# Performance work log

Measured on AMD Instinct MI355X. Metric: run time of the kernel, lower is better.

## Reference

```python
import jax, jax.numpy as jnp
import numpy as np

N_NODES = 10000
N_EDGES = 160000
HIDDEN = 64
NUM_RBF = 32
Q_DIM = 8
CUTOFF_UPPER = 5.0


def silu(x):
    return x * jax.nn.sigmoid(x)


def tensor_norm(X):
    # X: [n, 3, 3, H] -> [n, H] (Frobenius norm squared over the 3x3 dims)
    return (X * X).sum(axis=(1, 2))


def decompose_tensor(X):
    # X: [n, 3, 3, H] -> I: [n, H] (trace/3), A: antisym [n,3,3,H], S: sym traceless [n,3,3,H]
    eye = jnp.eye(3, dtype=X.dtype)[None, :, :, None]
    I = jnp.einsum('naah->nh', X) / 3.0
    Xt = X.transpose(0, 2, 1, 3)
    A = 0.5 * (X - Xt)
    S = 0.5 * (X + Xt) - I[:, None, None, :] * eye
    return I, A, S


def compose_tensor(I, A, S):
    eye = jnp.eye(3, dtype=A.dtype)[None, :, :, None]
    return I[:, None, None, :] * eye + A + S


def tmm(P, Q):
    # 3x3 matmul per (atom, channel): [n,3,3,H] x [n,3,3,H] -> [n,3,3,H]
    return jnp.einsum('nach,ncbh->nabh', P, Q)


def setup_inputs() -> dict:
    key = jax.random.key(0)
    ks = jax.random.split(key, 16)
    H = HIDDEN
    inp = {
        'X': jax.random.normal(ks[0], (N_NODES, 3, 3, H), jnp.float32),
        'charges': jax.random.normal(ks[1], (N_NODES, Q_DIM), jnp.float32),
        'edge_weight': jax.random.uniform(ks[2], (N_EDGES,), jnp.float32) * CUTOFF_UPPER,
        'edge_attr': jax.random.normal(ks[3], (N_EDGES, NUM_RBF), jnp.float32),
        'edge_index': jax.random.randint(ks[4], (2, N_EDGES), 0, N_NODES, jnp.int32),
    }
    d_in = NUM_RBF + 2 * Q_DIM
    inp['Ws1'] = jax.random.normal(ks[5], (d_in, H), jnp.float32) / np.sqrt(d_in).astype(np.float32)
    inp['bs1'] = jnp.zeros((H,), jnp.float32)
    inp['Ws2'] = jax.random.normal(ks[6], (H, 2 * H), jnp.float32) / np.sqrt(H).astype(np.float32)
    inp['bs2'] = jnp.zeros((2 * H,), jnp.float32)
    inp['Ws3'] = jax.random.normal(ks[7], (2 * H, 3 * H), jnp.float32) / np.sqrt(2 * H).astype(np.float32)
    inp['bs3'] = jnp.zeros((3 * H,), jnp.float32)
    for i in range(6):
        inp['Wt%d' % i] = jax.random.normal(ks[8 + i], (H, H), jnp.float32) / np.sqrt(H).astype(np.float32)
    return inp


def reference(X, charges, edge_weight, edge_attr, Ws1, bs1, Ws2, bs2, Ws3, bs3,
              Wt0, Wt1, Wt2, Wt3, Wt4, Wt5, edge_index):
    H = HIDDEN
    n = X.shape[0]
    row, col = edge_index[0], edge_index[1]
    # cosine cutoff (cutoff_lower = 0)
    C = 0.5 * (jnp.cos(edge_weight * (jnp.pi / CUTOFF_UPPER)) + 1.0)
    C = C * (edge_weight < CUTOFF_UPPER).astype(X.dtype)
    # edge scalar MLP on [rbf, q_i, q_j]
    h = jnp.concatenate([edge_attr, charges[row], charges[col]], axis=-1)
    h = silu(h @ Ws1 + bs1)
    h = silu(h @ Ws2 + bs2)
    h = silu(h @ Ws3 + bs3)
    w = (h * C[:, None]).reshape(h.shape[0], 3, H)  # [E, 3, H]
    # normalize node tensors
    X = X / (tensor_norm(X) + 1.0)[:, None, None, :]
    I, A, S = decompose_tensor(X)
    I = I @ Wt0
    A = A @ Wt1
    S = S @ Wt2
    Y = compose_tensor(I, A, S)
    # message passing: gather I/A/S at source (edge_index[1]), weight per component, scatter-add at dest (edge_index[0])
    eye = jnp.eye(3, dtype=X.dtype)[None, :, :, None]
    msg_e = ((w[:, 0] * I[col])[:, None, None, :] * eye
             + w[:, 1][:, None, None, :] * A[col]
             + w[:, 2][:, None, None, :] * S[col])  # [E, 3, 3, H]
    msg = jax.ops.segment_sum(msg_e, row, num_segments=n)  # [n, 3, 3, H]
    # O(3): C = msg @ Y + Y @ msg (3x3 matmul per channel)
    Cm = tmm(msg, Y) + tmm(Y, msg)
    I2, A2, S2 = decompose_tensor(Cm)
    normp1 = tensor_norm(Cm) + 1.0
    I2 = I2 / normp1
    A2 = A2 / normp1[:, None, None, :]
    S2 = S2 / normp1[:, None, None, :]
    I2 = I2 @ Wt3
    A2 = A2 @ Wt4
    S2 = S2 @ Wt5
    dX = compose_tensor(I2, A2, S2)
    return X + dX + tmm(dX, dX)
```

## Files before the change

### kernel.cpp

```cpp
#include <hip/hip_runtime.h>
#include <math.h>

#define HD 64

typedef _Float16 half8 __attribute__((ext_vector_type(8)));
typedef _Float16 half4v __attribute__((ext_vector_type(4)));
typedef float floatx4 __attribute__((ext_vector_type(4)));

__device__ __forceinline__ float silu_f(float x) {
    return x * __builtin_amdgcn_rcpf(1.0f + __expf(-x));
}

__global__ __launch_bounds__(256) void pre_wconv(
    const float* __restrict__ X,
    const float* __restrict__ Wt0, const float* __restrict__ Wt1, const float* __restrict__ Wt2,
    float* __restrict__ Tn, _Float16* __restrict__ TnH, int N, int nbPre,
    const float* __restrict__ Ws1, const float* __restrict__ Ws2, const float* __restrict__ Ws3,
    _Float16* __restrict__ W1f, _Float16* __restrict__ W2f, _Float16* __restrict__ W3f)
{
    if (blockIdx.x >= nbPre) {
        int id = (blockIdx.x - nbPre) * 256 + threadIdx.x;
        if (id < 4096) {
            int i = id & 7, l = (id >> 3) & 63, t = id >> 9;
            int s = t >> 2, nt = t & 3;
            int k = s * 32 + (l >> 4) * 8 + i;
            int n = nt * 16 + (l & 15);
            W1f[id] = (k < 48) ? (_Float16)Ws1[k * 64 + n] : (_Float16)0.f;
        } else if (id < 4096 + 8192) {
            int j = id - 4096;
            int i = j & 7, l = (j >> 3) & 63, t = j >> 9;
            int s = t >> 3, nt = t & 7;
            int k = s * 32 + (l >> 4) * 8 + i;
            int n = nt * 16 + (l & 15);
            W2f[j] = (_Float16)Ws2[k * 128 + n];
        } else if (id < 4096 + 8192 + 24576) {
            int j = id - 4096 - 8192;
            int i = j & 7, l = (j >> 3) & 63, t = j >> 9;
            int s = t / 12, nt = t % 12;
            int k = s * 32 + (l >> 4) * 8 + i;
            int n = nt * 16 + (l & 15);
            W3f[j] = (_Float16)Ws3[k * 192 + n];
        }
        return;
    }

    int sub = threadIdx.x >> 6;
    int h = threadIdx.x & 63;
    int n = blockIdx.x * 4 + sub;
    int nn = (n < N) ? n : (N - 1);

    const float* Xb = X + (size_t)nn * 9 * HD + h;
    float x[9];
    float nrm = 0.f;
#pragma unroll
    for (int i = 0; i < 9; ++i) { x[i] = Xb[i * HD]; nrm += x[i] * x[i]; }
    float inv = 1.0f / (nrm + 1.0f);
#pragma unroll
    for (int i = 0; i < 9; ++i) x[i] *= inv;

    float I0 = (x[0] + x[4] + x[8]) * (1.0f / 3.0f);
    __shared__ float comp[4][10][HD];
    comp[sub][0][h] = I0;
    comp[sub][1][h] = 0.5f * (x[1] - x[3]);
    comp[sub][2][h] = 0.5f * (x[2] - x[6]);
    comp[sub][3][h] = 0.5f * (x[5] - x[7]);
    comp[sub][4][h] = x[0] - I0;
    comp[sub][5][h] = 0.5f * (x[1] + x[3]);
    comp[sub][6][h] = 0.5f * (x[2] + x[6]);
    comp[sub][7][h] = x[4] - I0;
    comp[sub][8][h] = 0.5f * (x[5] + x[7]);
    comp[sub][9][h] = x[8] - I0;
    __syncthreads();
    float acc[10];
#pragma unroll
    for (int i = 0; i < 10; ++i) acc[i] = 0.f;
    for (int k = 0; k < HD; ++k) {
        float w0 = Wt0[k * HD + h];
        float w1 = Wt1[k * HD + h];
        float w2 = Wt2[k * HD + h];
        acc[0] += comp[sub][0][k] * w0;
        acc[1] += comp[sub][1][k] * w1;
        acc[2] += comp[sub][2][k] * w1;
        acc[3] += comp[sub][3][k] * w1;
#pragma unroll
        for (int j = 0; j < 6; ++j) acc[4 + j] += comp[sub][4 + j][k] * w2;
    }
    if (n < N) {
        float* tp = Tn + (size_t)n * 640 + h;
        _Float16* th = TnH + (size_t)n * 640 + h;
#pragma unroll
        for (int i = 0; i < 10; ++i) {
            tp[i * 64] = acc[i];
            th[i * 64] = (_Float16)acc[i];
        }
    }
}

__global__ __launch_bounds__(256) void count_kernel(
    const int* __restrict__ edge_index, int* __restrict__ cnt, int E)
{
    int e = blockIdx.x * 256 + threadIdx.x;
    if (e < E) atomicAdd(&cnt[edge_index[e]], 1);
}

__global__ __launch_bounds__(1024) void scanA(
    const int* __restrict__ cnt, int* __restrict__ offs, int* __restrict__ partial, int N)
{
    __shared__ int wsum[16];
    int tid = threadIdx.x, wid = tid >> 6, lane = tid & 63;
    int i = blockIdx.x * 1024 + tid;
    int v = (i < N) ? cnt[i] : 0;
    int s = v;
#pragma unroll
    for (int d = 1; d < 64; d <<= 1) {
        int t = __shfl_up(s, d, 64);
        if (lane >= d) s += t;
    }
    if (lane == 63) wsum[wid] = s;
    __syncthreads();
    if (tid == 0) {
        int run = 0;
#pragma unroll
        for (int w = 0; w < 16; ++w) { int t = wsum[w]; wsum[w] = run; run += t; }
        partial[blockIdx.x] = run;
    }
    __syncthreads();
    if (i < N) offs[i] = wsum[wid] + s - v;
}

__global__ __launch_bounds__(256) void scanC(
    int* __restrict__ offs, const int* __restrict__ partial, int* __restrict__ curs,
    int N, int E)
{
    int i = blockIdx.x * 256 + threadIdx.x;
    if (i < N) {
        int b = i >> 10;
        int basev = 0;
        for (int w = 0; w < b; ++w) basev += partial[w];
        int o = offs[i] + basev;
        offs[i] = o;
        curs[i] = o;
    }
    if (i == 0) offs[N] = E;
}

__global__ __launch_bounds__(256) void place_kernel(
    const int* __restrict__ edge_index, int* __restrict__ curs,
    int* __restrict__ rank, int* __restrict__ colP, int E)
{
    int e = blockIdx.x * 256 + threadIdx.x;
    if (e < E) {
        int p = atomicAdd(&curs[edge_index[e]], 1);
        rank[e] = p;
        colP[p] = edge_index[E + e];
    }
}

__global__ __launch_bounds__(256, 6) void mlp_mfma(
    const float* __restrict__ edge_attr, const float* __restrict__ charges,
    const float* __restrict__ edge_weight, const int* __restrict__ edge_index,
    const int* __restrict__ rank,
    const _Float16* __restrict__ W1f, const float* __restrict__ bs1,
    const _Float16* __restrict__ W2f, const float* __restrict__ bs2,
    const _Float16* __restrict__ W3f, const float* __restrict__ bs3,
    _Float16* __restrict__ bufH, int E)
{
    __shared__ __align__(16) _Float16 act[4][16][136];
    __shared__ float cvsS[4][16];
    __shared__ int rankSS[4][16];

    int tid = threadIdx.x;
    int wv = tid >> 6, l = tid & 63;
    int base = blockIdx.x * 64 + wv * 16;
    int row16 = l & 15, quad = l >> 4;

#pragma unroll
    for (int i = 0; i < 4; ++i) {
        int slot = l + i * 64;
        int e_l = slot >> 4, f = slot & 15;
        int e = base + e_l;
        int ee = (e < E) ? e : (E - 1);
        float4 v = make_float4(0.f, 0.f, 0.f, 0.f);
        if (f < 8) {
            v = *(const float4*)(edge_attr + (size_t)ee * 32 + f * 4);
        } else if (f < 10) {
            int r = edge_index[ee];
            v = *(const float4*)(charges + (size_t)r * 8 + (f - 8) * 4);
        } else if (f < 12) {
            int c = edge_index[E + ee];
            v = *(const float4*)(charges + (size_t)c * 8 + (f - 10) * 4);
        }
        half4v hv = { (_Float16)v.x, (_Float16)v.y, (_Float16)v.z, (_Float16)v.w };
        *(half4v*)&act[wv][e_l][f * 4] = hv;
    }
    if (l < 16) {
        int e = base + l;
        int ee = (e < E) ? e : (E - 1);
        rankSS[wv][l] = rank[ee];
        float wgt = edge_weight[ee];
        float cv = 0.5f * (__cosf(wgt * 0.6283185307179586f) + 1.0f);
        cvsS[wv][l] = (wgt < 5.0f) ? cv : 0.0f;
    }

    half8 A[2];
    A[0] = *(const half8*)&act[wv][row16][quad * 8];
    A[1] = *(const half8*)&act[wv][row16][32 + quad * 8];
    {
        half8 W[8];
#pragma unroll
        for (int t = 0; t < 8; ++t)
            W[t] = *(const half8*)(W1f + ((size_t)t * 64 + l) * 8);
        floatx4 acc1[4];
#pragma unroll
        for (int nt = 0; nt < 4; ++nt) {
            floatx4 c = {0.f, 0.f, 0.f, 0.f};
            c = __builtin_amdgcn_mfma_f32_16x16x32_f16(A[0], W[nt], c, 0, 0, 0);
            c = __builtin_amdgcn_mfma_f32_16x16x32_f16(A[1], W[4 + nt], c, 0, 0, 0);
            acc1[nt] = c;
        }
#pragma unroll
        for (int nt = 0; nt < 4; ++nt) {
            float b = bs1[nt * 16 + row16];
#pragma unroll
            for (int r = 0; r < 4; ++r)
                act[wv][quad * 4 + r][64 + nt * 16 + row16] = (_Float16)silu_f(acc1[nt][r] + b);
        }
    }

    A[0] = *(const half8*)&act[wv][row16][64 + quad * 8];
    A[1] = *(const half8*)&act[wv][row16][96 + quad * 8];
    {
        floatx4 acc2[8];
#pragma unroll
        for (int nt = 0; nt < 8; ++nt) acc2[nt] = (floatx4){0.f, 0.f, 0.f, 0.f};
#pragma unroll
        for (int s = 0; s < 2; ++s) {
            half8 W[8];
#pragma unroll
            for (int nt = 0; nt < 8; ++nt)
                W[nt] = *(const half8*)(W2f + ((size_t)(s * 8 + nt) * 64 + l) * 8);
#pragma unroll
            for (int nt = 0; nt < 8; ++nt)
                acc2[nt] = __builtin_amdgcn_mfma_f32_16x16x32_f16(A[s], W[nt], acc2[nt], 0, 0, 0);
        }
#pragma unroll
        for (int nt = 0; nt < 8; ++nt) {
            float b = bs2[nt * 16 + row16];
#pragma unroll
            for (int r = 0; r < 4; ++r)
                act[wv][quad * 4 + r][nt * 16 + row16] = (_Float16)silu_f(acc2[nt][r] + b);
        }
    }

    half8 A3[4];
#pragma unroll
    for (int s = 0; s < 4; ++s)
        A3[s] = *(const half8*)&act[wv][row16][s * 32 + quad * 8];

    float cvrow[4];
#pragma unroll
    for (int r = 0; r < 4; ++r) cvrow[r] = cvsS[wv][quad * 4 + r];

#pragma unroll
    for (int g = 0; g < 2; ++g) {
        floatx4 acc[4];
#pragma unroll
        for (int j = 0; j < 4; ++j) acc[j] = (floatx4){0.f, 0.f, 0.f, 0.f};
#pragma unroll
        for (int s = 0; s < 4; ++s) {
            half8 W[4];
#pragma unroll
            for (int j = 0; j < 4; ++j)
                W[j] = *(const half8*)(W3f + ((size_t)(s * 12 + g * 4 + j) * 64 + l) * 8);
#pragma unroll
            for (int j = 0; j < 4; ++j)
                acc[j] = __builtin_amdgcn_mfma_f32_16x16x32_f16(A3[s], W[j], acc[j], 0, 0, 0);
        }
#pragma unroll
        for (int j = 0; j < 4; ++j) {
            int nt = g * 4 + j;
            float b = bs3[nt * 16 + row16];
#pragma unroll
            for (int r = 0; r < 4; ++r)
                act[wv][quad * 4 + r][nt * 16 + row16] =
                    (_Float16)(silu_f(acc[j][r] + b) * cvrow[r]);
        }
    }
    {
        int fr = l >> 2;
        int ef = base + fr;
        if (ef < E) {
            _Float16* dst = bufH + (size_t)rankSS[wv][fr] * 192;
#pragma unroll
            for (int i = 0; i < 4; ++i) {
                int j = (l & 3) + i * 4;
                *(half8*)(dst + j * 8) = *(const half8*)&act[wv][fr][j * 8];
            }
        }
    }
    {
        floatx4 acc[4];
#pragma unroll
        for (int j = 0; j < 4; ++j) acc[j] = (floatx4){0.f, 0.f, 0.f, 0.f};
#pragma unroll
        for (int s = 0; s < 4; ++s) {
            half8 W[4];
#pragma unroll
            for (int j = 0; j < 4; ++j)
                W[j] = *(const half8*)(W3f + ((size_t)(s * 12 + 8 + j) * 64 + l) * 8);
#pragma unroll
            for (int j = 0; j < 4; ++j)
                acc[j] = __builtin_amdgcn_mfma_f32_16x16x32_f16(A3[s], W[j], acc[j], 0, 0, 0);
        }
#pragma unroll
        for (int j = 0; j < 4; ++j) {
            float b = bs3[(8 + j) * 16 + row16];
#pragma unroll
            for (int r = 0; r < 4; ++r)
                act[wv][quad * 4 + r][j * 16 + row16] =
                    (_Float16)(silu_f(acc[j][r] + b) * cvrow[r]);
        }
    }
    {
        int fr = l >> 2;
        int ef = base + fr;
        if (ef < E) {
            _Float16* dst = bufH + (size_t)rankSS[wv][fr] * 192;
#pragma unroll
            for (int i = 0; i < 2; ++i) {
                int j = (l & 3) + i * 4;
                *(half8*)(dst + (16 + j) * 8) = *(const half8*)&act[wv][fr][j * 8];
            }
        }
    }
}

__global__ __launch_bounds__(256) void msg_kernel(
    const _Float16* __restrict__ bufH, const int* __restrict__ colP,
    const int* __restrict__ offs, const _Float16* __restrict__ TnH,
    float* __restrict__ Mn, int N)
{
    __shared__ float part[4][10][64];
    int qtr = threadIdx.x >> 6;
    int lane = threadIdx.x & 63;
    int n = blockIdx.x;
    int beg = offs[n], end = offs[n + 1];
    int len = end - beg;
    int s0 = beg + (len * qtr) / 4;
    int s1 = beg + (len * (qtr + 1)) / 4;

    float a0 = 0.f, a1 = 0.f, a2 = 0.f, a3 = 0.f, a4 = 0.f;
    float a5 = 0.f, a6 = 0.f, a7 = 0.f, a8 = 0.f, a9 = 0.f;
#pragma unroll 2
    for (int idx = s0; idx < s1; ++idx) {
        int c = colP[idx];
        const _Float16* wp = bufH + (size_t)idx * 192;
        float w0 = (float)wp[lane];
        float w1 = (float)wp[64 + lane];
        float w2 = (float)wp[128 + lane];
        const _Float16* tp = TnH + (size_t)c * 640;
        a0 += w0 * (float)tp[lane];
        a1 += w1 * (float)tp[64 + lane];
        a2 += w1 * (float)tp[128 + lane];
        a3 += w1 * (float)tp[192 + lane];
        a4 += w2 * (float)tp[256 + lane];
        a5 += w2 * (float)tp[320 + lane];
        a6 += w2 * (float)tp[384 + lane];
        a7 += w2 * (float)tp[448 + lane];
        a8 += w2 * (float)tp[512 + lane];
        a9 += w2 * (float)tp[576 + lane];
    }
    part[qtr][0][lane] = a0; part[qtr][1][lane] = a1;
    part[qtr][2][lane] = a2; part[qtr][3][lane] = a3;
    part[qtr][4][lane] = a4; part[qtr][5][lane] = a5;
    part[qtr][6][lane] = a6; part[qtr][7][lane] = a7;
    part[qtr][8][lane] = a8; part[qtr][9][lane] = a9;
    __syncthreads();

    if (qtr < 2) {
        float* mp = Mn + (size_t)n * 640;
#pragma unroll
        for (int j = 0; j < 5; ++j) {
            int c = qtr * 5 + j;
            mp[c * 64 + lane] = (part[0][c][lane] + part[1][c][lane])
                              + (part[2][c][lane] + part[3][c][lane]);
        }
    }
}

__global__ __launch_bounds__(256) void node_post(
    const float* __restrict__ X,
    const float* __restrict__ Tn, const float* __restrict__ Mn,
    const float* __restrict__ Wt3, const float* __restrict__ Wt4, const float* __restrict__ Wt5,
    float* __restrict__ out, int N)
{
    int sub = threadIdx.x >> 6;
    int h = threadIdx.x & 63;
    int n = blockIdx.x * 4 + sub;
    int nn = (n < N) ? n : (N - 1);

    const float* Xb = X + (size_t)nn * 9 * HD + h;
    float x[9];
    float nr = 0.f;
#pragma unroll
    for (int i = 0; i < 9; ++i) { x[i] = Xb[i * HD]; nr += x[i] * x[i]; }
    float xinv = 1.0f / (nr + 1.0f);
#pragma unroll
    for (int i = 0; i < 9; ++i) x[i] *= xinv;

    const float* tp = Tn + (size_t)nn * 640 + h;
    const float* mp = Mn + (size_t)nn * 640 + h;
    float yI = tp[0], mI = mp[0];
    float yA[3], yS[6], mA[3], mS[6];
#pragma unroll
    for (int j = 0; j < 3; ++j) { yA[j] = tp[(1 + j) * 64]; mA[j] = mp[(1 + j) * 64]; }
#pragma unroll
    for (int j = 0; j < 6; ++j) { yS[j] = tp[(4 + j) * 64]; mS[j] = mp[(4 + j) * 64]; }

    float M[3][3] = {
        { mI + mS[0],     mA[0] + mS[1],   mA[1] + mS[2] },
        { -mA[0] + mS[1], mI + mS[3],      mA[2] + mS[4] },
        { -mA[1] + mS[2], -mA[2] + mS[4],  mI + mS[5] } };
    float Y[3][3] = {
        { yI + yS[0],     yA[0] + yS[1],   yA[1] + yS[2] },
        { -yA[0] + yS[1], yI + yS[3],      yA[2] + yS[4] },
        { -yA[1] + yS[2], -yA[2] + yS[4],  yI + yS[5] } };

    float Cm[3][3];
    float nrm = 0.f;
#pragma unroll
    for (int a = 0; a < 3; ++a) {
#pragma unroll
        for (int b = 0; b < 3; ++b) {
            float s = 0.f;
#pragma unroll
            for (int c = 0; c < 3; ++c) s += M[a][c] * Y[c][b] + Y[a][c] * M[c][b];
            Cm[a][b] = s;
            nrm += s * s;
        }
    }
    float inv = 1.0f / (nrm + 1.0f);
    float tr3 = (Cm[0][0] + Cm[1][1] + Cm[2][2]) * (1.0f / 3.0f);

    __shared__ float comp[4][10][HD];
    comp[sub][0][h] = tr3 * inv;
    comp[sub][1][h] = 0.5f * (Cm[0][1] - Cm[1][0]) * inv;
    comp[sub][2][h] = 0.5f * (Cm[0][2] - Cm[2][0]) * inv;
    comp[sub][3][h] = 0.5f * (Cm[1][2] - Cm[2][1]) * inv;
    comp[sub][4][h] = (Cm[0][0] - tr3) * inv;
    comp[sub][5][h] = 0.5f * (Cm[0][1] + Cm[1][0]) * inv;
    comp[sub][6][h] = 0.5f * (Cm[0][2] + Cm[2][0]) * inv;
    comp[sub][7][h] = (Cm[1][1] - tr3) * inv;
    comp[sub][8][h] = 0.5f * (Cm[1][2] + Cm[2][1]) * inv;
    comp[sub][9][h] = (Cm[2][2] - tr3) * inv;
    __syncthreads();

    float acc[10];
#pragma unroll
    for (int i = 0; i < 10; ++i) acc[i] = 0.f;
    for (int k = 0; k < HD; ++k) {
        float w3 = Wt3[k * HD + h];
        float w4 = Wt4[k * HD + h];
        float w5 = Wt5[k * HD + h];
        acc[0] += comp[sub][0][k] * w3;
        acc[1] += comp[sub][1][k] * w4;
        acc[2] += comp[sub][2][k] * w4;
        acc[3] += comp[sub][3][k] * w4;
#pragma unroll
        for (int j = 0; j < 6; ++j) acc[4 + j] += comp[sub][4 + j][k] * w5;
    }
    float D[3][3] = {
        { acc[0] + acc[4],  acc[1] + acc[5],  acc[2] + acc[6] },
        { -acc[1] + acc[5], acc[0] + acc[7],  acc[3] + acc[8] },
        { -acc[2] + acc[6], -acc[3] + acc[8], acc[0] + acc[9] } };

    if (n < N) {
        float* ob = out + (size_t)n * 9 * HD + h;
#pragma unroll
        for (int a = 0; a < 3; ++a) {
#pragma unroll
            for (int b = 0; b < 3; ++b) {
                float s = 0.f;
#pragma unroll
                for (int c = 0; c < 3; ++c) s += D[a][c] * D[c][b];
                ob[(a * 3 + b) * HD] = x[a * 3 + b] + D[a][b] + s;
            }
        }
    }
}

extern "C" void kernel_launch(void* const* d_in, const int* in_sizes, int n_in,
                              void* d_out, int out_size, void* d_ws, size_t ws_size,
                              hipStream_t stream)
{
    const float* X           = (const float*)d_in[0];
    const float* charges     = (const float*)d_in[1];
    const float* edge_weight = (const float*)d_in[2];
    const float* edge_attr   = (const float*)d_in[3];
    const int*   edge_index  = (const int*)d_in[4];
    const float* Ws1 = (const float*)d_in[5];
    const float* bs1 = (const float*)d_in[6];
    const float* Ws2 = (const float*)d_in[7];
    const float* bs2 = (const float*)d_in[8];
    const float* Ws3 = (const float*)d_in[9];
    const float* bs3 = (const float*)d_in[10];
    const float* Wt0 = (const float*)d_in[11];
    const float* Wt1 = (const float*)d_in[12];
    const float* Wt2 = (const float*)d_in[13];
    const float* Wt3 = (const float*)d_in[14];
    const float* Wt4 = (const float*)d_in[15];
    const float* Wt5 = (const float*)d_in[16];

    int N = in_sizes[0] / (9 * HD);
    int E = in_sizes[2];

    float* ws = (float*)d_ws;
    float* Tn  = ws;
    float* Mn  = Tn + (size_t)N * 640;
    _Float16* TnH  = (_Float16*)(Mn + (size_t)N * 640);
    _Float16* bufH = TnH + (size_t)N * 640;
    int* cnt   = (int*)(bufH + (size_t)E * 192);
    int* offs  = cnt + N;
    int* curs  = offs + N + 1;
    int* rank  = curs + N;
    int* colP  = rank + E;
    int* partial = colP + E;
    size_t fofs = ((size_t)((char*)(partial + 64) - (char*)d_ws) + 15) & ~(size_t)15;
    _Float16* W1f = (_Float16*)((char*)d_ws + fofs);
    _Float16* W2f = W1f + 4096;
    _Float16* W3f = W2f + 8192;

    hipMemsetAsync(cnt, 0, (size_t)N * sizeof(int), stream);

    int nbE256 = (E + 255) / 256;
    int nbN1024 = (N + 1023) / 1024;
    count_kernel<<<nbE256, 256, 0, stream>>>(edge_index, cnt, E);
    scanA<<<nbN1024, 1024, 0, stream>>>(cnt, offs, partial, N);
    scanC<<<(N + 255) / 256, 256, 0, stream>>>(offs, partial, curs, N, E);
    place_kernel<<<nbE256, 256, 0, stream>>>(edge_index, curs, rank, colP, E);

    int nbPre = (N + 3) / 4;
    pre_wconv<<<nbPre + 144, 256, 0, stream>>>(X, Wt0, Wt1, Wt2, Tn, TnH, N, nbPre,
                                               Ws1, Ws2, Ws3, W1f, W2f, W3f);

    int nbE64 = (E + 63) / 64;
    mlp_mfma<<<nbE64, 256, 0, stream>>>(edge_attr, charges, edge_weight, edge_index,
                                        rank, W1f, bs1, W2f, bs2, W3f, bs3, bufH, E);

    msg_kernel<<<N, 256, 0, stream>>>(bufH, colP, offs, TnH, Mn, N);

    node_post<<<(N + 3) / 4, 256, 0, stream>>>(X, Tn, Mn, Wt3, Wt4, Wt5, (float*)d_out, N);
}
```

Before: 171.6 us.

## Share edge tile across waves and split MLP output columns per wave

Restructures the edge MLP kernel so the four waves of a block share one 64-edge activation tile in LDS. Each wave now computes a slice of output columns for all 64 edges, instead of all columns for its own 16 edges. Each wave therefore loads only its slice of the weight fragments, which cuts global/L2 weight traffic and register pressure per wave. The cost is several block-wide barriers between layers and a larger LDS footprint, so the occupancy hint drops from 6 to 5.

```diff
diff --git a/kernel.cpp b/kernel.cpp
--- a/kernel.cpp
+++ b/kernel.cpp
@@ -156,7 +156,7 @@
     }
 }
 
-__global__ __launch_bounds__(256, 6) void mlp_mfma(
+__global__ __launch_bounds__(256, 5) void mlp_mfma(
     const float* __restrict__ edge_attr, const float* __restrict__ charges,
     const float* __restrict__ edge_weight, const int* __restrict__ edge_index,
     const int* __restrict__ rank,
@@ -165,18 +165,18 @@
     const _Float16* __restrict__ W3f, const float* __restrict__ bs3,
     _Float16* __restrict__ bufH, int E)
 {
-    __shared__ __align__(16) _Float16 act[4][16][136];
-    __shared__ float cvsS[4][16];
-    __shared__ int rankSS[4][16];
+    __shared__ __align__(16) _Float16 act[64][200];
+    __shared__ float cvsS[64];
+    __shared__ int rankSS[64];
 
     int tid = threadIdx.x;
     int wv = tid >> 6, l = tid & 63;
-    int base = blockIdx.x * 64 + wv * 16;
+    int base = blockIdx.x * 64;
     int row16 = l & 15, quad = l >> 4;
 
 #pragma unroll
     for (int i = 0; i < 4; ++i) {
-        int slot = l + i * 64;
+        int slot = tid + i * 256;
         int e_l = slot >> 4, f = slot & 15;
         int e = base + e_l;
         int ee = (e < E) ? e : (E - 1);
@@ -191,145 +191,122 @@
             v = *(const float4*)(charges + (size_t)c * 8 + (f - 10) * 4);
         }
         half4v hv = { (_Float16)v.x, (_Float16)v.y, (_Float16)v.z, (_Float16)v.w };
-        *(half4v*)&act[wv][e_l][f * 4] = hv;
-    }
-    if (l < 16) {
-        int e = base + l;
+        *(half4v*)&act[e_l][f * 4] = hv;
+    }
+    if (tid < 64) {
+        int e = base + tid;
         int ee = (e < E) ? e : (E - 1);
-        rankSS[wv][l] = rank[ee];
+        rankSS[tid] = rank[ee];
         float wgt = edge_weight[ee];
         float cv = 0.5f * (__cosf(wgt * 0.6283185307179586f) + 1.0f);
-        cvsS[wv][l] = (wgt < 5.0f) ? cv : 0.0f;
-    }
-
-    half8 A[2];
-    A[0] = *(const half8*)&act[wv][row16][quad * 8];
-    A[1] = *(const half8*)&act[wv][row16][32 + quad * 8];
+        cvsS[tid] = (wgt < 5.0f) ? cv : 0.0f;
+    }
+    __syncthreads();
+
     {
-        half8 W[8];
-#pragma unroll
-        for (int t = 0; t < 8; ++t)
-            W[t] = *(const half8*)(W1f + ((size_t)t * 64 + l) * 8);
+        half8 w0 = *(const half8*)(W1f + ((size_t)(0 * 4 + wv) * 64 + l) * 8);
+        half8 w1 = *(const half8*)(W1f + ((size_t)(1 * 4 + wv) * 64 + l) * 8);
         floatx4 acc1[4];
 #pragma unroll
-        for (int nt = 0; nt < 4; ++nt) {
+        for (int m = 0; m < 4; ++m) {
             floatx4 c = {0.f, 0.f, 0.f, 0.f};
-            c = __builtin_amdgcn_mfma_f32_16x16x32_f16(A[0], W[nt], c, 0, 0, 0);
-            c = __builtin_amdgcn_mfma_f32_16x16x32_f16(A[1], W[4 + nt], c, 0, 0, 0);
-            acc1[nt] = c;
-        }
-#pragma unroll
-        for (int nt = 0; nt < 4; ++nt) {
-            float b = bs1[nt * 16 + row16];
+            c = __builtin_amdgcn_mfma_f32_16x16x32_f16(
+                    *(const half8*)&act[m * 16 + row16][quad * 8], w0, c, 0, 0, 0);
+            c = __builtin_amdgcn_mfma_f32_16x16x32_f16(
+                    *(const half8*)&act[m * 16 + row16][32 + quad * 8], w1, c, 0, 0, 0);
+            acc1[m] = c;
+        }
+        __syncthreads();
+        float b = bs1[wv * 16 + row16];
+#pragma unroll
+        for (int m = 0; m < 4; ++m)
 #pragma unroll
             for (int r = 0; r < 4; ++r)
-                act[wv][quad * 4 + r][64 + nt * 16 + row16] = (_Float16)silu_f(acc1[nt][r] + b);
-        }
-    }
-
-    A[0] = *(const half8*)&act[wv][row16][64 + quad * 8];
-    A[1] = *(const half8*)&act[wv][row16][96 + quad * 8];
+                act[m * 16 + quad * 4 + r][128 + wv * 16 + row16] =
+                    (_Float16)silu_f(acc1[m][r] + b);
+    }
+    __syncthreads();
+
     {
-        floatx4 acc2[8];
-#pragma unroll
-        for (int nt = 0; nt < 8; ++nt) acc2[nt] = (floatx4){0.f, 0.f, 0.f, 0.f};
+        floatx4 acc2[4][2];
+#pragma unroll
+        for (int m = 0; m < 4; ++m)
+#pragma unroll
+            for (int j = 0; j < 2; ++j) acc2[m][j] = (floatx4){0.f, 0.f, 0.f, 0.f};
 #pragma unroll
         for (int s = 0; s < 2; ++s) {
-            half8 W[8];
-#pragma unroll
-            for (int nt = 0; nt < 8; ++nt)
-                W[nt] = *(const half8*)(W2f + ((size_t)(s * 8 + nt) * 64 + l) * 8);
-#pragma unroll
-            for (int nt = 0; nt < 8; ++nt)
-                acc2[nt] = __builtin_amdgcn_mfma_f32_16x16x32_f16(A[s], W[nt], acc2[nt], 0, 0, 0);
-        }
-#pragma unroll
-        for (int nt = 0; nt < 8; ++nt) {
-            float b = bs2[nt * 16 + row16];
-#pragma unroll
-            for (int r = 0; r < 4; ++r)
-                act[wv][quad * 4 + r][nt * 16 + row16] = (_Float16)silu_f(acc2[nt][r] + b);
-        }
-    }
-
-    half8 A3[4];
-#pragma unroll
-    for (int s = 0; s < 4; ++s)
-        A3[s] = *(const half8*)&act[wv][row16][s * 32 + quad * 8];
-
-    float cvrow[4];
-#pragma unroll
-    for (int r = 0; r < 4; ++r) cvrow[r] = cvsS[wv][quad * 4 + r];
-
-#pragma unroll
-    for (int g = 0; g < 2; ++g) {
-        floatx4 acc[4];
-#pragma unroll
-        for (int j = 0; j < 4; ++j) acc[j] = (floatx4){0.f, 0.f, 0.f, 0.f};
-#pragma unroll
-        for (int s = 0; s < 4; ++s) {
-            half8 W[4];
-#pragma unroll
-            for (int j = 0; j < 4; ++j)
-                W[j] = *(const half8*)(W3f + ((size_t)(s * 12 + g * 4 + j) * 64 + l) * 8);
-#pragma unroll
-            for (int j = 0; j < 4; ++j)
-                acc[j] = __builtin_amdgcn_mfma_f32_16x16x32_f16(A3[s], W[j], acc[j], 0, 0, 0);
-        }
-#pragma unroll
-        for (int j = 0; j < 4; ++j) {
-            int nt = g * 4 + j;
-            float b = bs3[nt * 16 + row16];
-#pragma unroll
-            for (int r = 0; r < 4; ++r)
-                act[wv][quad * 4 + r][nt * 16 + row16] =
-                    (_Float16)(silu_f(acc[j][r] + b) * cvrow[r]);
-        }
-    }
+            half8 w0 = *(const half8*)(W2f + ((size_t)(s * 8 + wv * 2 + 0) * 64 + l) * 8);
+            half8 w1 = *(const half8*)(W2f + ((size_t)(s * 8 + wv * 2 + 1) * 64 + l) * 8);
+#pragma unroll
+            for (int m = 0; m < 4; ++m) {
+                half8 a = *(const half8*)&act[m * 16 + row16][128 + s * 32 + quad * 8];
+                acc2[m][0] = __builtin_amdgcn_mfma_f32_16x16x32_f16(a, w0, acc2[m][0], 0, 0, 0);
+                acc2[m][1] = __builtin_amdgcn_mfma_f32_16x16x32_f16(a, w1, acc2[m][1], 0, 0, 0);
+            }
+        }
+        float b0 = bs2[(wv * 2 + 0) * 16 + row16];
+        float b1 = bs2[(wv * 2 + 1) * 16 + row16];
+#pragma unroll
+        for (int m = 0; m < 4; ++m)
+#pragma unroll
+            for (int r = 0; r < 4; ++r) {
+                act[m * 16 + quad * 4 + r][(wv * 2 + 0) * 16 + row16] =
+                    (_Float16)silu_f(acc2[m][0][r] + b0);
+                act[m * 16 + quad * 4 + r][(wv * 2 + 1) * 16 + row16] =
+                    (_Float16)silu_f(acc2[m][1][r] + b1);
+            }
+    }
+    __syncthreads();
+
+    floatx4 acc3[4][3];
+#pragma unroll
+    for (int m = 0; m < 4; ++m)
+#pragma unroll
+        for (int j = 0; j < 3; ++j) acc3[m][j] = (floatx4){0.f, 0.f, 0.f, 0.f};
+#pragma unroll
+    for (int s = 0; s < 4; ++s) {
+        half8 w0 = *(const half8*)(W3f + ((size_t)(s * 12 + wv * 3 + 0) * 64 + l) * 8);
+        half8 w1 = *(const half8*)(W3f + ((size_t)(s * 12 + wv * 3 + 1) * 64 + l) * 8);
+        half8 w2 = *(const half8*)(W3f + ((size_t)(s * 12 + wv * 3 + 2) * 64 + l) * 8);
+#pragma unroll
+        for (int m = 0; m < 4; ++m) {
+            half8 a = *(const half8*)&act[m * 16 + row16][s * 32 + quad * 8];
+            acc3[m][0] = __builtin_amdgcn_mfma_f32_16x16x32_f16(a, w0, acc3[m][0], 0, 0, 0);
+            acc3[m][1] = __builtin_amdgcn_mfma_f32_16x16x32_f16(a, w1, acc3[m][1], 0, 0, 0);
+            acc3[m][2] = __builtin_amdgcn_mfma_f32_16x16x32_f16(a, w2, acc3[m][2], 0, 0, 0);
+        }
+    }
+    __syncthreads();
+
     {
-        int fr = l >> 2;
+        float b0 = bs3[(wv * 3 + 0) * 16 + row16];
+        float b1 = bs3[(wv * 3 + 1) * 16 + row16];
+        float b2 = bs3[(wv * 3 + 2) * 16 + row16];
+#pragma unroll
+        for (int m = 0; m < 4; ++m) {
+#pragma unroll
+            for (int r = 0; r < 4; ++r) {
+                float cv = cvsS[m * 16 + quad * 4 + r];
+                act[m * 16 + quad * 4 + r][(wv * 3 + 0) * 16 + row16] =
+                    (_Float16)(silu_f(acc3[m][0][r] + b0) * cv);
+                act[m * 16 + quad * 4 + r][(wv * 3 + 1) * 16 + row16] =
+                    (_Float16)(silu_f(acc3[m][1][r] + b1) * cv);
+                act[m * 16 + quad * 4 + r][(wv * 3 + 2) * 16 + row16] =
+                    (_Float16)(silu_f(acc3[m][2][r] + b2) * cv);
+            }
+        }
+    }
+    __syncthreads();
+
+    {
+        int fr = tid >> 2;
         int ef = base + fr;
         if (ef < E) {
-            _Float16* dst = bufH + (size_t)rankSS[wv][fr] * 192;
-#pragma unroll
-            for (int i = 0; i < 4; ++i) {
-                int j = (l & 3) + i * 4;
-                *(half8*)(dst + j * 8) = *(const half8*)&act[wv][fr][j * 8];
-            }
-        }
-    }
-    {
-        floatx4 acc[4];
-#pragma unroll
-        for (int j = 0; j < 4; ++j) acc[j] = (floatx4){0.f, 0.f, 0.f, 0.f};
-#pragma unroll
-        for (int s = 0; s < 4; ++s) {
-            half8 W[4];
-#pragma unroll
-            for (int j = 0; j < 4; ++j)
-                W[j] = *(const half8*)(W3f + ((size_t)(s * 12 + 8 + j) * 64 + l) * 8);
-#pragma unroll
-            for (int j = 0; j < 4; ++j)
-                acc[j] = __builtin_amdgcn_mfma_f32_16x16x32_f16(A3[s], W[j], acc[j], 0, 0, 0);
-        }
-#pragma unroll
-        for (int j = 0; j < 4; ++j) {
-            float b = bs3[(8 + j) * 16 + row16];
-#pragma unroll
-            for (int r = 0; r < 4; ++r)
-                act[wv][quad * 4 + r][j * 16 + row16] =
-                    (_Float16)(silu_f(acc[j][r] + b) * cvrow[r]);
-        }
-    }
-    {
-        int fr = l >> 2;
-        int ef = base + fr;
-        if (ef < E) {
-            _Float16* dst = bufH + (size_t)rankSS[wv][fr] * 192;
-#pragma unroll
-            for (int i = 0; i < 2; ++i) {
-                int j = (l & 3) + i * 4;
-                *(half8*)(dst + (16 + j) * 8) = *(const half8*)&act[wv][fr][j * 8];
+            _Float16* dst = bufH + (size_t)rankSS[fr] * 192;
+#pragma unroll
+            for (int i = 0; i < 6; ++i) {
+                int j = (tid & 3) + i * 4;
+                *(half8*)(dst + j * 8) = *(const half8*)&act[fr][j * 8];
             }
         }
     }
```

Result: faster. 166.7 us (-2.9%).
